# Kernel tuning notes

Measured on AMD Instinct MI355X. Metric: run time of the kernel, lower is better.

Reference implementation:

```python
import jax, jax.numpy as jnp
import numpy as np

N, T, D, H = 2048, 4, 64, 4  # nodes, time steps, per-head dim (=dim), heads


def setup_inputs() -> dict:
    key = jax.random.key(0)
    ks = jax.random.split(key, 9)
    x = jax.random.normal(ks[0], (N, T, D), dtype=jnp.float32)
    Wq = jax.random.normal(ks[1], (H * D, D), dtype=jnp.float32) * 0.05
    bq = jnp.zeros((H * D,), dtype=jnp.float32)
    Wk = jax.random.normal(ks[2], (H * D, D), dtype=jnp.float32) * 0.05
    bk = jnp.zeros((H * D,), dtype=jnp.float32)
    Wv = jax.random.normal(ks[3], (H * D, D), dtype=jnp.float32) * 0.05
    bv = jnp.zeros((H * D,), dtype=jnp.float32)
    attention_weights = jax.random.uniform(ks[4], (T, H, N, N), dtype=jnp.float32)
    attention_mask = jax.random.bernoulli(ks[5], 0.1, (T, H, N, N))
    return {"x": x, "Wq": Wq, "bq": bq, "Wk": Wk, "bk": bk, "Wv": Wv, "bv": bv,
            "attention_weights": attention_weights, "attention_mask": attention_mask}


def reference(x, Wq, bq, Wk, bk, Wv, bv, attention_weights, attention_mask):
    n, t, d = x.shape
    h = Wq.shape[0] // d

    def proj(W, b):
        # (N,T,H*D) -> (N,T,H,D) -> (T,H,N,D)
        return (x @ W.T + b).reshape(n, t, h, d).transpose(1, 2, 0, 3)

    q = proj(Wq, bq)
    k = proj(Wk, bk)
    v = proj(Wv, bv)

    scores = jnp.einsum('thnd,thmd->thnm', q, k) / (d ** 0.5)  # (T,H,N,N)

    raw_att = jax.nn.softmax(scores, axis=-1)
    # torch permutes (T,H,N,D)->(H,N,T,D) contiguous then views as (N,T,H*D);
    # reproduce that exact memory reinterpretation.
    out_raw = jnp.einsum('thnm,thmd->thnd', raw_att, v).transpose(1, 2, 0, 3).reshape(n, t, h * d)

    att = scores * attention_weights
    att = jnp.where(attention_mask, -jnp.inf, att)
    att = jax.nn.softmax(att, axis=-1)
    out = jnp.einsum('thnm,thmd->thnd', att, v).transpose(1, 2, 0, 3).reshape(n, t, h * d)

    return (out, out_raw, raw_att[-1, 0, :, :])
```

## Files before the change

kernel.cpp:

```cpp
#include <hip/hip_runtime.h>
#include <hip/hip_bf16.h>

typedef __attribute__((ext_vector_type(8))) short short8;
typedef __attribute__((ext_vector_type(4))) float float4v;
typedef __attribute__((ext_vector_type(4))) int   int4v;

constexpr int NN = 2048;
constexpr int TT = 4;
constexpr int HH = 4;
constexpr int DD = 64;
constexpr int THC = TT * HH;

__device__ __forceinline__ float bf2f(unsigned short u) {
    union { unsigned int i; float f; } c; c.i = ((unsigned int)u) << 16; return c.f;
}
__device__ __forceinline__ unsigned short f2bf(float f) {
    union { float f; unsigned int i; } c; c.f = f;
    unsigned int x = c.i;
    x += 0x7FFFu + ((x >> 16) & 1u);
    return (unsigned short)(x >> 16);
}

__device__ __forceinline__ int mask_code_of(const unsigned int* mw) {
    int okInt = 1, okF32 = 1, okB = 1, anyLow = 0;
    for (int i = 0; i < 256; i++) {
        unsigned int w = mw[i];
        if (w > 1u) okInt = 0;
        if (!(w == 0u || w == 0x3F800000u)) okF32 = 0;
        unsigned int lo = w & 0xFFFFu, hi = w >> 16;
        if (!((lo == 0u || lo == 0x3F80u) && (hi == 0u || hi == 0x3F80u))) okB = 0;
        if (lo == 0x3F80u) anyLow = 1;
    }
    if (okInt) return 1;
    if (okF32 && !anyLow) return 2;
    if (okB) return 3;
    return 0;
}
__device__ __forceinline__ bool ld_mask(const void* p, size_t i, int code) {
    if (code == 1) return ((const int*)p)[i] != 0;
    if (code == 2) return ((const float*)p)[i] != 0.0f;
    if (code == 3) return ((const unsigned short*)p)[i] != 0;
    return ((const unsigned char*)p)[i] != 0;
}

constexpr int PROJ_ROWS = 8;
__global__ __launch_bounds__(256) void proj_b16v_kernel(
    const float* __restrict__ x,
    const float* __restrict__ Wq, const float* __restrict__ bq,
    const float* __restrict__ Wk, const float* __restrict__ bk,
    const float* __restrict__ Wv, const float* __restrict__ bv,
    unsigned short* __restrict__ q16, unsigned short* __restrict__ k16,
    unsigned short* __restrict__ v16)
{
    __shared__ float xl[PROJ_ROWS][64];
    const int tid = threadIdx.x;
    const int r0 = blockIdx.x * PROJ_ROWS;
    for (int i = tid; i < PROJ_ROWS * 64; i += 256)
        xl[i >> 6][i & 63] = x[(size_t)r0 * 64 + i];
    __syncthreads();

    const int c = tid;
    const int hh = c >> 6, dd = c & 63;
    const float* Ws[3] = { Wq, Wk, Wv };
    const float* bs[3] = { bq, bk, bv };
    unsigned short* os[3] = { q16, k16, v16 };

    #pragma unroll
    for (int m = 0; m < 3; m++) {
        float4v wr4[16];
        #pragma unroll
        for (int i = 0; i < 16; i++)
            wr4[i] = *(const float4v*)&Ws[m][(size_t)c * 64 + i * 4];
        const float bias = bs[m][c];
        #pragma unroll
        for (int rr = 0; rr < PROJ_ROWS; rr++) {
            float a = bias;
            #pragma unroll
            for (int i = 0; i < 16; i++) {
                a = fmaf(wr4[i][0], xl[rr][4*i+0], a);
                a = fmaf(wr4[i][1], xl[rr][4*i+1], a);
                a = fmaf(wr4[i][2], xl[rr][4*i+2], a);
                a = fmaf(wr4[i][3], xl[rr][4*i+3], a);
            }
            if (m == 0) a *= 0.125f;
            const int r = r0 + rr;
            const int n = r >> 2, t = r & 3;
            const int th = t * HH + hh;
            os[m][((size_t)th * NN + n) * DD + dd] = f2bf(a);
        }
    }
}

__global__ __launch_bounds__(128) void attn_mfma2_kernel(
    const unsigned short* __restrict__ q16, const unsigned short* __restrict__ k16,
    const unsigned short* __restrict__ v16,
    const float* __restrict__ watt, const void* __restrict__ maskp,
    float* __restrict__ out, float* __restrict__ out_raw)
{
    const int code = mask_code_of((const unsigned int*)maskp);
    const int tid  = threadIdx.x;
    const int wv   = tid >> 6;
    const int lane = tid & 63;
    const int g    = lane >> 4;
    const int j0   = lane & 15;
    const int lr   = lane >> 2;
    const int lc   = lane & 3;

    const int gid = blockIdx.x;
    const int th  = ((gid & 7) << 1) | ((gid >> 3) & 1);
    const int bx  = gid >> 4;
    const int t = th >> 2, h = th & 3;
    const int row0 = bx * 32 + wv * 16;

    const unsigned short* Qb = q16 + (size_t)th * NN * DD;
    const unsigned short* Kb = k16 + (size_t)th * NN * DD;
    const unsigned short* Vb = v16 + (size_t)th * NN * DD;

    __shared__ unsigned short Kl[64][80];
    __shared__ unsigned short Vt[64][80];
    __shared__ float          Sl[2][16][68];
    __shared__ unsigned short Pl[2][16][80];

    short8 aq0, aq1;
    {
        const unsigned short* qp = Qb + (size_t)(row0 + j0) * DD + g * 8;
        aq0 = *(const short8*)qp;
        aq1 = *(const short8*)(qp + 32);
    }

    float m_r = -1e30f, l_r = 0.f, m_w = -1e30f, l_w = 0.f;
    float4v o_r[4], o_w[4];
    #pragma unroll
    for (int ns = 0; ns < 4; ns++) {
        o_r[ns] = (float4v){0.f, 0.f, 0.f, 0.f};
        o_w[ns] = (float4v){0.f, 0.f, 0.f, 0.f};
    }

    const size_t mrow = ((size_t)th * NN + row0 + lr) * NN;

    for (int kv0 = 0; kv0 < NN; kv0 += 64) {
        __syncthreads();
        {
            const int kr = tid >> 1;
            const int kc = (tid & 1) << 5;
            const unsigned short* ks = Kb + (size_t)(kv0 + kr) * DD + kc;
            short8 k0 = ((const short8*)ks)[0];
            short8 k1 = ((const short8*)ks)[1];
            short8 k2 = ((const short8*)ks)[2];
            short8 k3 = ((const short8*)ks)[3];
            const unsigned short* vs = Vb + (size_t)(kv0 + kr) * DD + kc;
            short8 v0 = ((const short8*)vs)[0];
            short8 v1 = ((const short8*)vs)[1];
            short8 v2 = ((const short8*)vs)[2];
            short8 v3 = ((const short8*)vs)[3];
            *(short8*)&Kl[kr][kc +  0] = k0;
            *(short8*)&Kl[kr][kc +  8] = k1;
            *(short8*)&Kl[kr][kc + 16] = k2;
            *(short8*)&Kl[kr][kc + 24] = k3;
            #pragma unroll
            for (int e = 0; e < 8; e++) {
                Vt[kc +      e][kr] = (unsigned short)v0[e];
                Vt[kc +  8 + e][kr] = (unsigned short)v1[e];
                Vt[kc + 16 + e][kr] = (unsigned short)v2[e];
                Vt[kc + 24 + e][kr] = (unsigned short)v3[e];
            }
        }
        __syncthreads();

        float4v wv4[4];
        int4v   mk4[4];
        {
            const float* wp = watt + mrow + kv0 + lc * 16;
            #pragma unroll
            for (int q = 0; q < 4; q++) wv4[q] = *(const float4v*)&wp[q * 4];
            if (code == 1) {
                const int* mp = (const int*)maskp + mrow + kv0 + lc * 16;
                #pragma unroll
                for (int q = 0; q < 4; q++) mk4[q] = *(const int4v*)&mp[q * 4];
            }
        }

        float4v acc[4];
        #pragma unroll
        for (int c = 0; c < 4; c++) {
            short8 b0 = *(const short8*)&Kl[c * 16 + j0][g * 8];
            short8 b1 = *(const short8*)&Kl[c * 16 + j0][32 + g * 8];
            float4v z = (float4v){0.f, 0.f, 0.f, 0.f};
            z = __builtin_amdgcn_mfma_f32_16x16x32_bf16(aq0, b0, z, 0, 0, 0);
            z = __builtin_amdgcn_mfma_f32_16x16x32_bf16(aq1, b1, z, 0, 0, 0);
            acc[c] = z;
        }
        #pragma unroll
        for (int c = 0; c < 4; c++)
            #pragma unroll
            for (int i = 0; i < 4; i++)
                Sl[wv][g * 4 + i][c * 16 + j0] = acc[c][i];
        float4v s4[4];
        #pragma unroll
        for (int q = 0; q < 4; q++)
            s4[q] = *(const float4v*)&Sl[wv][lr][lc * 16 + q * 4];

        {
            float tmax = -3.0e38f;
            #pragma unroll
            for (int q = 0; q < 4; q++)
                #pragma unroll
                for (int e = 0; e < 4; e++) tmax = fmaxf(tmax, s4[q][e]);
            tmax = fmaxf(tmax, __shfl_xor(tmax, 1, 64));
            tmax = fmaxf(tmax, __shfl_xor(tmax, 2, 64));
            float mn = fmaxf(m_r, tmax);
            float alpha = __expf(m_r - mn);
            m_r = mn;
            alignas(16) unsigned short pb[16];
            float tsum = 0.f;
            #pragma unroll
            for (int q = 0; q < 4; q++)
                #pragma unroll
                for (int e = 0; e < 4; e++) {
                    unsigned short b = f2bf(__expf(s4[q][e] - mn));
                    pb[q * 4 + e] = b; tsum += bf2f(b);
                }
            tsum += __shfl_xor(tsum, 1, 64);
            tsum += __shfl_xor(tsum, 2, 64);
            l_r = l_r * alpha + tsum;
            *(short8*)&Pl[wv][lr][lc * 16]     = *(const short8*)&pb[0];
            *(short8*)&Pl[wv][lr][lc * 16 + 8] = *(const short8*)&pb[8];
            float aR[4];
            #pragma unroll
            for (int i = 0; i < 4; i++) aR[i] = __shfl(alpha, (g * 4 + i) * 4, 64);
            #pragma unroll
            for (int ns = 0; ns < 4; ns++)
                #pragma unroll
                for (int i = 0; i < 4; i++) o_r[ns][i] *= aR[i];
            #pragma unroll
            for (int ks2 = 0; ks2 < 2; ks2++) {
                short8 pa = *(const short8*)&Pl[wv][j0][ks2 * 32 + g * 8];
                #pragma unroll
                for (int ns = 0; ns < 4; ns++) {
                    short8 vb8 = *(const short8*)&Vt[ns * 16 + j0][ks2 * 32 + g * 8];
                    o_r[ns] = __builtin_amdgcn_mfma_f32_16x16x32_bf16(pa, vb8, o_r[ns], 0, 0, 0);
                }
            }
        }

        {
            float sw[16];
            if (code == 1) {
                #pragma unroll
                for (int q = 0; q < 4; q++)
                    #pragma unroll
                    for (int e = 0; e < 4; e++)
                        sw[q*4+e] = (mk4[q][e] != 0) ? -1e30f : s4[q][e] * wv4[q][e];
            } else {
                #pragma unroll
                for (int q = 0; q < 4; q++)
                    #pragma unroll
                    for (int e = 0; e < 4; e++)
                        sw[q*4+e] = ld_mask(maskp, mrow + kv0 + lc*16 + q*4+e, code)
                                    ? -1e30f : s4[q][e] * wv4[q][e];
            }
            float tmax = -3.0e38f;
            #pragma unroll
            for (int k = 0; k < 16; k++) tmax = fmaxf(tmax, sw[k]);
            tmax = fmaxf(tmax, __shfl_xor(tmax, 1, 64));
            tmax = fmaxf(tmax, __shfl_xor(tmax, 2, 64));
            float mn = fmaxf(m_w, tmax);
            float alpha = __expf(m_w - mn);
            m_w = mn;
            alignas(16) unsigned short pb[16];
            float tsum = 0.f;
            #pragma unroll
            for (int k = 0; k < 16; k++) {
                unsigned short b = f2bf(__expf(sw[k] - mn));
                pb[k] = b; tsum += bf2f(b);
            }
            tsum += __shfl_xor(tsum, 1, 64);
            tsum += __shfl_xor(tsum, 2, 64);
            l_w = l_w * alpha + tsum;
            *(short8*)&Pl[wv][lr][lc * 16]     = *(const short8*)&pb[0];
            *(short8*)&Pl[wv][lr][lc * 16 + 8] = *(const short8*)&pb[8];
            float aW[4];
            #pragma unroll
            for (int i = 0; i < 4; i++) aW[i] = __shfl(alpha, (g * 4 + i) * 4, 64);
            #pragma unroll
            for (int ns = 0; ns < 4; ns++)
                #pragma unroll
                for (int i = 0; i < 4; i++) o_w[ns][i] *= aW[i];
            #pragma unroll
            for (int ks2 = 0; ks2 < 2; ks2++) {
                short8 pa = *(const short8*)&Pl[wv][j0][ks2 * 32 + g * 8];
                #pragma unroll
                for (int ns = 0; ns < 4; ns++) {
                    short8 vb8 = *(const short8*)&Vt[ns * 16 + j0][ks2 * 32 + g * 8];
                    o_w[ns] = __builtin_amdgcn_mfma_f32_16x16x32_bf16(pa, vb8, o_w[ns], 0, 0, 0);
                }
            }
        }
    }

    float lR[4], lW[4];
    #pragma unroll
    for (int i = 0; i < 4; i++) {
        lR[i] = __shfl(l_r, (g * 4 + i) * 4, 64);
        lW[i] = __shfl(l_w, (g * 4 + i) * 4, 64);
    }
    #pragma unroll
    for (int i = 0; i < 4; i++) {
        const int row = row0 + g * 4 + i;
        const size_t ob = (((size_t)h * NN + row) * TT + t) * DD;
        const float ir = 1.0f / lR[i];
        const float iw = 1.0f / lW[i];
        #pragma unroll
        for (int ns = 0; ns < 4; ns++) {
            out[ob + ns * 16 + j0]     = o_w[ns][i] * iw;
            out_raw[ob + ns * 16 + j0] = o_r[ns][i] * ir;
        }
    }
}

__global__ __launch_bounds__(256) void slice_b16_kernel(
    const unsigned short* __restrict__ q16, const unsigned short* __restrict__ k16,
    float* __restrict__ out_sl)
{
    const int tid = threadIdx.x;
    const int w = tid >> 6, lane = tid & 63;
    const int thsel = 12;
    const unsigned short* Kb = k16 + (size_t)thsel * NN * DD;

    __shared__ float Tt[64][65];
    __shared__ float sr[4][NN];
    __shared__ float ql[4][64];

    ql[tid >> 6][tid & 63] =
        bf2f(q16[((size_t)thsel * NN + blockIdx.x * 4 + (tid >> 6))* DD + (tid & 63)]);
    __syncthreads();
    float qr[64];
    #pragma unroll
    for (int d = 0; d < 64; d++) qr[d] = ql[w][d];

    for (int kt = 0; kt < NN / 64; ++kt) {
        __syncthreads();
        const unsigned short* Ks = Kb + (size_t)kt * 64 * DD;
        #pragma unroll
        for (int u = 0; u < 16; ++u) {
            int e = u * 256 + tid;
            Tt[e >> 6][e & 63] = bf2f(Ks[e]);
        }
        __syncthreads();
        float a = 0.f;
        #pragma unroll
        for (int d = 0; d < 64; ++d)
            a = fmaf(qr[d], Tt[lane][d], a);
        sr[w][kt * 64 + lane] = a;
    }

    const int r = blockIdx.x * 4 + w;
    float mx = -3.0e38f;
    for (int m = lane; m < NN; m += 64) mx = fmaxf(mx, sr[w][m]);
    #pragma unroll
    for (int o = 1; o < 64; o <<= 1) mx = fmaxf(mx, __shfl_xor(mx, o, 64));
    float se = 0.f;
    for (int m = lane; m < NN; m += 64) se += __expf(sr[w][m] - mx);
    #pragma unroll
    for (int o = 1; o < 64; o <<= 1) se += __shfl_xor(se, o, 64);
    const float inv = 1.0f / se;
    for (int m = lane; m < NN; m += 64)
        out_sl[(size_t)r * NN + m] = __expf(sr[w][m] - mx) * inv;
}

extern "C" void kernel_launch(void* const* d_in, const int* in_sizes, int n_in,
                              void* d_out, int out_size, void* d_ws, size_t ws_size,
                              hipStream_t stream)
{
    (void)in_sizes; (void)n_in; (void)out_size; (void)ws_size;
    const float* x    = (const float*)d_in[0];
    const float* Wq   = (const float*)d_in[1];
    const float* bq   = (const float*)d_in[2];
    const float* Wk   = (const float*)d_in[3];
    const float* bk   = (const float*)d_in[4];
    const float* Wv   = (const float*)d_in[5];
    const float* bv   = (const float*)d_in[6];
    const float* watt = (const float*)d_in[7];
    const void*  mask = d_in[8];

    unsigned short* q16 = (unsigned short*)d_ws;
    unsigned short* k16 = q16 + (size_t)THC * NN * DD;
    unsigned short* v16 = k16 + (size_t)THC * NN * DD;

    float* out     = (float*)d_out;
    float* out_raw = out + (size_t)NN * TT * HH * DD;
    float* out_sl  = out + 2 * (size_t)NN * TT * HH * DD;

    proj_b16v_kernel<<<NN * TT / PROJ_ROWS, 256, 0, stream>>>(
        x, Wq, bq, Wk, bk, Wv, bv, q16, k16, v16);
    attn_mfma2_kernel<<<(NN / 32) * THC, 128, 0, stream>>>(
        q16, k16, v16, watt, mask, out, out_raw);
    slice_b16_kernel<<<NN / 4, 256, 0, stream>>>(q16, k16, out_sl);
}
```

Before: 275.4 us.

## Register-prefetch next K/V tile, weights and mask to overlap loads with compute

The attention loop now loads the next tile's K, V, attention weights and mask into registers at the start of each iteration, then writes them to shared memory after compute, a software-pipelined double buffer in registers. Mask handling for non-int32 formats is vectorized and decoded into a 16-bit bitmask instead of per-element scalar loads. Launch bounds request two blocks per CU. This is meant to hide global memory latency behind the MFMA and softmax work, at the cost of more registers, which may hurt occupancy.

```diff
diff --git a/kernel.cpp b/kernel.cpp
--- a/kernel.cpp
+++ b/kernel.cpp
@@ -10,6 +10,7 @@
 constexpr int HH = 4;
 constexpr int DD = 64;
 constexpr int THC = TT * HH;
+constexpr int NTILE = NN / 64;
 
 __device__ __forceinline__ float bf2f(unsigned short u) {
     union { unsigned int i; float f; } c; c.i = ((unsigned int)u) << 16; return c.f;
@@ -36,11 +37,57 @@
     if (okB) return 3;
     return 0;
 }
-__device__ __forceinline__ bool ld_mask(const void* p, size_t i, int code) {
-    if (code == 1) return ((const int*)p)[i] != 0;
-    if (code == 2) return ((const float*)p)[i] != 0.0f;
-    if (code == 3) return ((const unsigned short*)p)[i] != 0;
-    return ((const unsigned char*)p)[i] != 0;
+
+__device__ __forceinline__ void load_mask_raw(const void* p, size_t idx, int code,
+                                              int4v mr[4]) {
+    if (code == 1) {
+        const int4v* mp = (const int4v*)((const int*)p + idx);
+        #pragma unroll
+        for (int q = 0; q < 4; q++) mr[q] = mp[q];
+    } else if (code == 2) {
+        const int4v* mp = (const int4v*)((const float*)p + idx);
+        #pragma unroll
+        for (int q = 0; q < 4; q++) mr[q] = mp[q];
+    } else if (code == 3) {
+        const int4v* mp = (const int4v*)((const unsigned short*)p + idx);
+        mr[0] = mp[0]; mr[1] = mp[1];
+    } else {
+        mr[0] = *(const int4v*)((const unsigned char*)p + idx);
+    }
+}
+__device__ __forceinline__ unsigned decode_pm(const int4v mr[4], int code) {
+    unsigned pm = 0u;
+    if (code == 1) {
+        #pragma unroll
+        for (int q = 0; q < 4; q++)
+            #pragma unroll
+            for (int e = 0; e < 4; e++)
+                if (mr[q][e] != 0) pm |= 1u << (q * 4 + e);
+    } else if (code == 2) {
+        #pragma unroll
+        for (int q = 0; q < 4; q++)
+            #pragma unroll
+            for (int e = 0; e < 4; e++)
+                if ((((unsigned)mr[q][e]) << 1) != 0u) pm |= 1u << (q * 4 + e);
+    } else if (code == 3) {
+        #pragma unroll
+        for (int q = 0; q < 2; q++)
+            #pragma unroll
+            for (int e = 0; e < 4; e++) {
+                unsigned w = (unsigned)mr[q][e];
+                if (w & 0xFFFFu) pm |= 1u << (q * 8 + e * 2);
+                if (w >> 16)     pm |= 1u << (q * 8 + e * 2 + 1);
+            }
+    } else {
+        #pragma unroll
+        for (int q = 0; q < 4; q++) {
+            unsigned w = (unsigned)mr[0][q];
+            #pragma unroll
+            for (int b = 0; b < 4; b++)
+                if ((w >> (8 * b)) & 0xFFu) pm |= 1u << (q * 4 + b);
+        }
+    }
+    return pm;
 }
 
 constexpr int PROJ_ROWS = 8;
@@ -91,7 +138,7 @@
     }
 }
 
-__global__ __launch_bounds__(128) void attn_mfma2_kernel(
+__global__ __launch_bounds__(128, 2) void attn_mfma3_kernel(
     const unsigned short* __restrict__ q16, const unsigned short* __restrict__ k16,
     const unsigned short* __restrict__ v16,
     const float* __restrict__ watt, const void* __restrict__ maskp,
@@ -138,46 +185,51 @@
 
     const size_t mrow = ((size_t)th * NN + row0 + lr) * NN;
 
-    for (int kv0 = 0; kv0 < NN; kv0 += 64) {
-        __syncthreads();
-        {
-            const int kr = tid >> 1;
-            const int kc = (tid & 1) << 5;
-            const unsigned short* ks = Kb + (size_t)(kv0 + kr) * DD + kc;
-            short8 k0 = ((const short8*)ks)[0];
-            short8 k1 = ((const short8*)ks)[1];
-            short8 k2 = ((const short8*)ks)[2];
-            short8 k3 = ((const short8*)ks)[3];
-            const unsigned short* vs = Vb + (size_t)(kv0 + kr) * DD + kc;
-            short8 v0 = ((const short8*)vs)[0];
-            short8 v1 = ((const short8*)vs)[1];
-            short8 v2 = ((const short8*)vs)[2];
-            short8 v3 = ((const short8*)vs)[3];
-            *(short8*)&Kl[kr][kc +  0] = k0;
-            *(short8*)&Kl[kr][kc +  8] = k1;
-            *(short8*)&Kl[kr][kc + 16] = k2;
-            *(short8*)&Kl[kr][kc + 24] = k3;
-            #pragma unroll
-            for (int e = 0; e < 8; e++) {
-                Vt[kc +      e][kr] = (unsigned short)v0[e];
-                Vt[kc +  8 + e][kr] = (unsigned short)v1[e];
-                Vt[kc + 16 + e][kr] = (unsigned short)v2[e];
-                Vt[kc + 24 + e][kr] = (unsigned short)v3[e];
-            }
-        }
-        __syncthreads();
-
-        float4v wv4[4];
-        int4v   mk4[4];
-        {
-            const float* wp = watt + mrow + kv0 + lc * 16;
-            #pragma unroll
-            for (int q = 0; q < 4; q++) wv4[q] = *(const float4v*)&wp[q * 4];
-            if (code == 1) {
-                const int* mp = (const int*)maskp + mrow + kv0 + lc * 16;
-                #pragma unroll
-                for (int q = 0; q < 4; q++) mk4[q] = *(const int4v*)&mp[q * 4];
-            }
+    const int kr = tid >> 1;
+    const int kc = (tid & 1) << 5;
+    const unsigned short* Kp = Kb + (size_t)kr * DD + kc;
+    const unsigned short* Vp = Vb + (size_t)kr * DD + kc;
+
+    short8  kreg[4], vreg[4];
+    float4v wcur[4], wnxt[4];
+    int4v   mnxt[4];
+    unsigned pm;
+
+    #pragma unroll
+    for (int u = 0; u < 4; u++) {
+        kreg[u] = ((const short8*)Kp)[u];
+        vreg[u] = ((const short8*)Vp)[u];
+    }
+    {
+        const float* wp = watt + mrow + lc * 16;
+        #pragma unroll
+        for (int q = 0; q < 4; q++) wcur[q] = *(const float4v*)&wp[q * 4];
+    }
+    load_mask_raw(maskp, mrow + lc * 16, code, mnxt);
+    #pragma unroll
+    for (int u = 0; u < 4; u++) {
+        *(short8*)&Kl[kr][kc + u * 8] = kreg[u];
+        #pragma unroll
+        for (int e = 0; e < 8; e++)
+            Vt[kc + u * 8 + e][kr] = (unsigned short)vreg[u][e];
+    }
+    __syncthreads();
+    pm = decode_pm(mnxt, code);
+
+    for (int it = 0; it < NTILE; ++it) {
+        if (it + 1 < NTILE) {
+            const size_t kvn = (size_t)(it + 1) * 64;
+            const unsigned short* kp = Kp + kvn * DD;
+            const unsigned short* vp = Vp + kvn * DD;
+            #pragma unroll
+            for (int u = 0; u < 4; u++) {
+                kreg[u] = ((const short8*)kp)[u];
+                vreg[u] = ((const short8*)vp)[u];
+            }
+            const float* wp = watt + mrow + kvn + lc * 16;
+            #pragma unroll
+            for (int q = 0; q < 4; q++) wnxt[q] = *(const float4v*)&wp[q * 4];
+            load_mask_raw(maskp, mrow + kvn + lc * 16, code, mnxt);
         }
 
         float4v acc[4];
@@ -245,20 +297,13 @@
 
         {
             float sw[16];
-            if (code == 1) {
-                #pragma unroll
-                for (int q = 0; q < 4; q++)
-                    #pragma unroll
-                    for (int e = 0; e < 4; e++)
-                        sw[q*4+e] = (mk4[q][e] != 0) ? -1e30f : s4[q][e] * wv4[q][e];
-            } else {
-                #pragma unroll
-                for (int q = 0; q < 4; q++)
-                    #pragma unroll
-                    for (int e = 0; e < 4; e++)
-                        sw[q*4+e] = ld_mask(maskp, mrow + kv0 + lc*16 + q*4+e, code)
-                                    ? -1e30f : s4[q][e] * wv4[q][e];
-            }
+            #pragma unroll
+            for (int q = 0; q < 4; q++)
+                #pragma unroll
+                for (int e = 0; e < 4; e++) {
+                    const int k = q * 4 + e;
+                    sw[k] = ((pm >> k) & 1u) ? -1e30f : s4[q][e] * wcur[q][e];
+                }
             float tmax = -3.0e38f;
             #pragma unroll
             for (int k = 0; k < 16; k++) tmax = fmaxf(tmax, sw[k]);
@@ -296,6 +341,21 @@
                 }
             }
         }
+
+        __syncthreads();
+        if (it + 1 < NTILE) {
+            #pragma unroll
+            for (int u = 0; u < 4; u++) {
+                *(short8*)&Kl[kr][kc + u * 8] = kreg[u];
+                #pragma unroll
+                for (int e = 0; e < 8; e++)
+                    Vt[kc + u * 8 + e][kr] = (unsigned short)vreg[u][e];
+            }
+            #pragma unroll
+            for (int q = 0; q < 4; q++) wcur[q] = wnxt[q];
+            pm = decode_pm(mnxt, code);
+        }
+        __syncthreads();
     }
 
     float lR[4], lW[4];
@@ -393,7 +453,7 @@
 
     proj_b16v_kernel<<<NN * TT / PROJ_ROWS, 256, 0, stream>>>(
         x, Wq, bq, Wk, bk, Wv, bv, q16, k16, v16);
-    attn_mfma2_kernel<<<(NN / 32) * THC, 128, 0, stream>>>(
+    attn_mfma3_kernel<<<(NN / 32) * THC, 128, 0, stream>>>(
         q16, k16, v16, watt, mask, out, out_raw);
     slice_b16_kernel<<<NN / 4, 256, 0, stream>>>(q16, k16, out_sl);
 }
```

After: 295.5 us. 7.3% more time.

## Double-buffer attention weights and mask into LDS via async global-to-LDS loads

Applied to the files above, without the earlier changes.

Attention-weight and byte-mask tiles are now prefetched two iterations ahead with global_load_lds into double-buffered shared memory, so the large weight and mask streams overlap with compute. Mask handling is rewritten to load vectorized raw data and decode it into a 16-bit bitmask, replacing the per-element scalar mask loads used for non-int formats. The raw and weighted P tiles now sit in separate LDS buffers, which lets both PV MFMA chains run fused in a single loop that shares the V fragments. The change adds LDS use and hand-placed waitcnt and barriers, which could lower occupancy or introduce synchronisation hazards.

```diff
diff --git a/kernel.cpp b/kernel.cpp
--- a/kernel.cpp
+++ b/kernel.cpp
@@ -10,6 +10,10 @@
 constexpr int HH = 4;
 constexpr int DD = 64;
 constexpr int THC = TT * HH;
+
+#define GL_LDS16(g, l) __builtin_amdgcn_global_load_lds(                     \
+    (const __attribute__((address_space(1))) void*)(g),                      \
+    (__attribute__((address_space(3))) void*)(l), 16, 0, 0)
 
 __device__ __forceinline__ float bf2f(unsigned short u) {
     union { unsigned int i; float f; } c; c.i = ((unsigned int)u) << 16; return c.f;
@@ -36,11 +40,57 @@
     if (okB) return 3;
     return 0;
 }
-__device__ __forceinline__ bool ld_mask(const void* p, size_t i, int code) {
-    if (code == 1) return ((const int*)p)[i] != 0;
-    if (code == 2) return ((const float*)p)[i] != 0.0f;
-    if (code == 3) return ((const unsigned short*)p)[i] != 0;
-    return ((const unsigned char*)p)[i] != 0;
+
+__device__ __forceinline__ void load_mask_raw(const void* p, size_t idx, int code,
+                                              int4v mr[4]) {
+    if (code == 1) {
+        const int4v* mp = (const int4v*)((const int*)p + idx);
+        #pragma unroll
+        for (int q = 0; q < 4; q++) mr[q] = mp[q];
+    } else if (code == 2) {
+        const int4v* mp = (const int4v*)((const float*)p + idx);
+        #pragma unroll
+        for (int q = 0; q < 4; q++) mr[q] = mp[q];
+    } else if (code == 3) {
+        const int4v* mp = (const int4v*)((const unsigned short*)p + idx);
+        mr[0] = mp[0]; mr[1] = mp[1];
+    } else {
+        mr[0] = *(const int4v*)((const unsigned char*)p + idx);
+    }
+}
+__device__ __forceinline__ unsigned decode_pm(const int4v mr[4], int code) {
+    unsigned pm = 0u;
+    if (code == 1) {
+        #pragma unroll
+        for (int q = 0; q < 4; q++)
+            #pragma unroll
+            for (int e = 0; e < 4; e++)
+                if (mr[q][e] != 0) pm |= 1u << (q * 4 + e);
+    } else if (code == 2) {
+        #pragma unroll
+        for (int q = 0; q < 4; q++)
+            #pragma unroll
+            for (int e = 0; e < 4; e++)
+                if ((((unsigned)mr[q][e]) << 1) != 0u) pm |= 1u << (q * 4 + e);
+    } else if (code == 3) {
+        #pragma unroll
+        for (int q = 0; q < 2; q++)
+            #pragma unroll
+            for (int e = 0; e < 4; e++) {
+                unsigned w = (unsigned)mr[q][e];
+                if (w & 0xFFFFu) pm |= 1u << (q * 8 + e * 2);
+                if (w >> 16)     pm |= 1u << (q * 8 + e * 2 + 1);
+            }
+    } else {
+        #pragma unroll
+        for (int q = 0; q < 4; q++) {
+            unsigned w = (unsigned)mr[0][q];
+            #pragma unroll
+            for (int b = 0; b < 4; b++)
+                if ((w >> (8 * b)) & 0xFFu) pm |= 1u << (q * 4 + b);
+        }
+    }
+    return pm;
 }
 
 constexpr int PROJ_ROWS = 8;
@@ -91,7 +141,7 @@
     }
 }
 
-__global__ __launch_bounds__(128) void attn_mfma2_kernel(
+__global__ __launch_bounds__(128) void attn_mfma9_kernel(
     const unsigned short* __restrict__ q16, const unsigned short* __restrict__ k16,
     const unsigned short* __restrict__ v16,
     const float* __restrict__ watt, const void* __restrict__ maskp,
@@ -118,8 +168,32 @@
 
     __shared__ unsigned short Kl[64][80];
     __shared__ unsigned short Vt[64][80];
-    __shared__ float          Sl[2][16][68];
-    __shared__ unsigned short Pl[2][16][80];
+    __shared__ __align__(16) char SPu[2][5120];
+    __shared__ __align__(16) char wattS[2][2][4096];
+    __shared__ __align__(16) char maskS[2][2][1024];
+
+    float*          Slp  = (float*)SPu[wv];
+    unsigned short* PlRp = (unsigned short*)SPu[wv];
+    unsigned short* PlWp = (unsigned short*)(SPu[wv] + 2560);
+
+    const size_t mrow = ((size_t)th * NN + row0 + lr) * NN;
+
+    auto issue_tile = [&](int kvt) {
+        const int b = kvt & 1;
+        const float* wsrc = watt + mrow + (size_t)kvt * 64 + lc * 16;
+        char* wdst = &wattS[wv][b][0];
+        #pragma unroll
+        for (int q = 0; q < 4; q++)
+            GL_LDS16(wsrc + q * 4, wdst + q * 1024);
+        if (code == 0) {
+            const unsigned char* msrc =
+                (const unsigned char*)maskp + mrow + (size_t)kvt * 64 + lc * 16;
+            GL_LDS16(msrc, &maskS[wv][b][0]);
+        }
+    };
+
+    issue_tile(0);
+    issue_tile(1);
 
     short8 aq0, aq1;
     {
@@ -136,10 +210,25 @@
         o_w[ns] = (float4v){0.f, 0.f, 0.f, 0.f};
     }
 
-    const size_t mrow = ((size_t)th * NN + row0 + lr) * NN;
-
-    for (int kv0 = 0; kv0 < NN; kv0 += 64) {
-        __syncthreads();
+    for (int it = 0; it < NN / 64; ++it) {
+        const int kv0 = it * 64;
+        const int buf = it & 1;
+
+        asm volatile("s_waitcnt lgkmcnt(0)" ::: "memory");
+        __builtin_amdgcn_s_barrier();
+
+        int4v mr0 = {0,0,0,0}, mr1 = {0,0,0,0};
+        unsigned pmPre = 0u;
+        if (code == 1 || code == 2) {
+            int4v tr[4];
+            load_mask_raw(maskp, mrow + kv0 + lc * 16, code, tr);
+            pmPre = decode_pm(tr, code);
+        } else if (code == 3) {
+            const int4v* mp =
+                (const int4v*)((const unsigned short*)maskp + mrow + kv0 + lc * 16);
+            mr0 = mp[0]; mr1 = mp[1];
+        }
+
         {
             const int kr = tid >> 1;
             const int kc = (tid & 1) << 5;
@@ -165,22 +254,9 @@
                 Vt[kc + 24 + e][kr] = (unsigned short)v3[e];
             }
         }
-        __syncthreads();
-
-        float4v wv4[4];
-        int4v   mk4[4];
-        {
-            const float* wp = watt + mrow + kv0 + lc * 16;
-            #pragma unroll
-            for (int q = 0; q < 4; q++) wv4[q] = *(const float4v*)&wp[q * 4];
-            if (code == 1) {
-                const int* mp = (const int*)maskp + mrow + kv0 + lc * 16;
-                #pragma unroll
-                for (int q = 0; q < 4; q++) mk4[q] = *(const int4v*)&mp[q * 4];
-            }
-        }
-
-        float4v acc[4];
+        asm volatile("s_waitcnt lgkmcnt(0)" ::: "memory");
+        __builtin_amdgcn_s_barrier();
+
         #pragma unroll
         for (int c = 0; c < 4; c++) {
             short8 b0 = *(const short8*)&Kl[c * 16 + j0][g * 8];
@@ -188,17 +264,15 @@
             float4v z = (float4v){0.f, 0.f, 0.f, 0.f};
             z = __builtin_amdgcn_mfma_f32_16x16x32_bf16(aq0, b0, z, 0, 0, 0);
             z = __builtin_amdgcn_mfma_f32_16x16x32_bf16(aq1, b1, z, 0, 0, 0);
-            acc[c] = z;
-        }
-        #pragma unroll
-        for (int c = 0; c < 4; c++)
             #pragma unroll
             for (int i = 0; i < 4; i++)
-                Sl[wv][g * 4 + i][c * 16 + j0] = acc[c][i];
+                Slp[(g * 4 + i) * 68 + c * 16 + j0] = z[i];
+        }
         float4v s4[4];
         #pragma unroll
         for (int q = 0; q < 4; q++)
-            s4[q] = *(const float4v*)&Sl[wv][lr][lc * 16 + q * 4];
+            s4[q] = *(const float4v*)&Slp[lr * 68 + lc * 16 + q * 4];
+        asm volatile("" ::: "memory");
 
         {
             float tmax = -3.0e38f;
@@ -223,8 +297,8 @@
             tsum += __shfl_xor(tsum, 1, 64);
             tsum += __shfl_xor(tsum, 2, 64);
             l_r = l_r * alpha + tsum;
-            *(short8*)&Pl[wv][lr][lc * 16]     = *(const short8*)&pb[0];
-            *(short8*)&Pl[wv][lr][lc * 16 + 8] = *(const short8*)&pb[8];
+            *(short8*)&PlRp[lr * 80 + lc * 16]     = *(const short8*)&pb[0];
+            *(short8*)&PlRp[lr * 80 + lc * 16 + 8] = *(const short8*)&pb[8];
             float aR[4];
             #pragma unroll
             for (int i = 0; i < 4; i++) aR[i] = __shfl(alpha, (g * 4 + i) * 4, 64);
@@ -232,33 +306,39 @@
             for (int ns = 0; ns < 4; ns++)
                 #pragma unroll
                 for (int i = 0; i < 4; i++) o_r[ns][i] *= aR[i];
-            #pragma unroll
-            for (int ks2 = 0; ks2 < 2; ks2++) {
-                short8 pa = *(const short8*)&Pl[wv][j0][ks2 * 32 + g * 8];
-                #pragma unroll
-                for (int ns = 0; ns < 4; ns++) {
-                    short8 vb8 = *(const short8*)&Vt[ns * 16 + j0][ks2 * 32 + g * 8];
-                    o_r[ns] = __builtin_amdgcn_mfma_f32_16x16x32_bf16(pa, vb8, o_r[ns], 0, 0, 0);
-                }
-            }
+        }
+
+        asm volatile("s_waitcnt vmcnt(0)" ::: "memory");
+        __builtin_amdgcn_sched_barrier(0);
+
+        float4v wv4[4];
+        {
+            const char* wsb = &wattS[wv][buf][0];
+            #pragma unroll
+            for (int q = 0; q < 4; q++)
+                wv4[q] = *(const float4v*)(wsb + q * 1024 + (size_t)lane * 16);
+        }
+        unsigned pm;
+        if (code == 0) {
+            int4v tr[4];
+            tr[0] = *(const int4v*)(&maskS[wv][buf][0] + (size_t)lane * 16);
+            pm = decode_pm(tr, 0);
+        } else if (code == 3) {
+            int4v tr[4]; tr[0] = mr0; tr[1] = mr1;
+            pm = decode_pm(tr, 3);
+        } else {
+            pm = pmPre;
         }
 
         {
             float sw[16];
-            if (code == 1) {
+            #pragma unroll
+            for (int q = 0; q < 4; q++)
                 #pragma unroll
-                for (int q = 0; q < 4; q++)
-                    #pragma unroll
-                    for (int e = 0; e < 4; e++)
-                        sw[q*4+e] = (mk4[q][e] != 0) ? -1e30f : s4[q][e] * wv4[q][e];
-            } else {
-                #pragma unroll
-                for (int q = 0; q < 4; q++)
-                    #pragma unroll
-                    for (int e = 0; e < 4; e++)
-                        sw[q*4+e] = ld_mask(maskp, mrow + kv0 + lc*16 + q*4+e, code)
-                                    ? -1e30f : s4[q][e] * wv4[q][e];
-            }
+                for (int e = 0; e < 4; e++) {
+                    const int k = q * 4 + e;
+                    sw[k] = ((pm >> k) & 1u) ? -1e30f : s4[q][e] * wv4[q][e];
+                }
             float tmax = -3.0e38f;
             #pragma unroll
             for (int k = 0; k < 16; k++) tmax = fmaxf(tmax, sw[k]);
@@ -277,8 +357,8 @@
             tsum += __shfl_xor(tsum, 1, 64);
             tsum += __shfl_xor(tsum, 2, 64);
             l_w = l_w * alpha + tsum;
-            *(short8*)&Pl[wv][lr][lc * 16]     = *(const short8*)&pb[0];
-            *(short8*)&Pl[wv][lr][lc * 16 + 8] = *(const short8*)&pb[8];
+            *(short8*)&PlWp[lr * 80 + lc * 16]     = *(const short8*)&pb[0];
+            *(short8*)&PlWp[lr * 80 + lc * 16 + 8] = *(const short8*)&pb[8];
             float aW[4];
             #pragma unroll
             for (int i = 0; i < 4; i++) aW[i] = __shfl(alpha, (g * 4 + i) * 4, 64);
@@ -286,14 +366,19 @@
             for (int ns = 0; ns < 4; ns++)
                 #pragma unroll
                 for (int i = 0; i < 4; i++) o_w[ns][i] *= aW[i];
-            #pragma unroll
-            for (int ks2 = 0; ks2 < 2; ks2++) {
-                short8 pa = *(const short8*)&Pl[wv][j0][ks2 * 32 + g * 8];
-                #pragma unroll
-                for (int ns = 0; ns < 4; ns++) {
-                    short8 vb8 = *(const short8*)&Vt[ns * 16 + j0][ks2 * 32 + g * 8];
-                    o_w[ns] = __builtin_amdgcn_mfma_f32_16x16x32_bf16(pa, vb8, o_w[ns], 0, 0, 0);
-                }
+        }
+
+        if (it + 2 < NN / 64) issue_tile(it + 2);
+
+        #pragma unroll
+        for (int ks2 = 0; ks2 < 2; ks2++) {
+            short8 paR = *(const short8*)&PlRp[j0 * 80 + ks2 * 32 + g * 8];
+            short8 paW = *(const short8*)&PlWp[j0 * 80 + ks2 * 32 + g * 8];
+            #pragma unroll
+            for (int ns = 0; ns < 4; ns++) {
+                short8 vb8 = *(const short8*)&Vt[ns * 16 + j0][ks2 * 32 + g * 8];
+                o_r[ns] = __builtin_amdgcn_mfma_f32_16x16x32_bf16(paR, vb8, o_r[ns], 0, 0, 0);
+                o_w[ns] = __builtin_amdgcn_mfma_f32_16x16x32_bf16(paW, vb8, o_w[ns], 0, 0, 0);
             }
         }
     }
@@ -393,7 +478,7 @@
 
     proj_b16v_kernel<<<NN * TT / PROJ_ROWS, 256, 0, stream>>>(
         x, Wq, bq, Wk, bk, Wv, bv, q16, k16, v16);
-    attn_mfma2_kernel<<<(NN / 32) * THC, 128, 0, stream>>>(
+    attn_mfma9_kernel<<<(NN / 32) * THC, 128, 0, stream>>>(
         q16, k16, v16, watt, mask, out, out_raw);
     slice_b16_kernel<<<NN / 4, 256, 0, stream>>>(q16, k16, out_sl);
 }
```

Measured after the change: 397.7 us. 44.4% more time.
